# Performance work log

Hardware: AMD Instinct MI355X
Metric: run time of the kernel (lower is better)

Reference implementation:

```python
import jax, jax.numpy as jnp
import numpy as np

TEMP = 0.5
EPS_NORM = 1e-12  # F.normalize clamp eps
EPS_ROW = 1e-8


def _l2_normalize(x):
    n = jnp.sqrt(jnp.sum(x * x, axis=1, keepdims=True))
    return x / jnp.maximum(n, EPS_NORM)


def _sim(z1, z2):
    # exp(cosine_sim / T), [N, N]
    z1 = _l2_normalize(z1)
    z2 = _l2_normalize(z2)
    return jnp.exp(jnp.matmul(z1, z2.T) / TEMP)


def _loss_term(mat, pos):
    row = mat / (jnp.sum(mat, axis=1, keepdims=True) + EPS_ROW)
    return -jnp.mean(jnp.log(jnp.sum(row * pos, axis=-1)))


def setup_inputs() -> dict:
    key = jax.random.key(0)
    k1, k2, k3 = jax.random.split(key, 3)
    N, D = 8192, 64
    z_mp = jax.random.normal(k1, (N, D), dtype=jnp.float32)
    z_sc = jax.random.normal(k2, (N, D), dtype=jnp.float32)
    # sparse binary positive mask with guaranteed self-positives on diagonal
    pos = (jax.random.uniform(k3, (N, N)) < 0.005).astype(jnp.float32)
    pos = jnp.maximum(pos, jnp.eye(N, dtype=jnp.float32))
    return {"z_mp": z_mp, "z_sc": z_sc, "pos": pos}


def reference(z_mp, z_sc, pos):
    m_mp2sc = _sim(z_mp, z_sc)        # [N, N]
    m_sc2mp = m_mp2sc.T               # [N, N]
    m_mp2mp = _sim(z_mp, z_mp)        # [N, N]
    m_sc2sc = _sim(z_sc, z_sc)        # [N, N]
    loss = (_loss_term(m_mp2sc, pos)
            + _loss_term(m_sc2mp, pos)
            + _loss_term(m_mp2mp, pos)
            + _loss_term(m_sc2sc, pos))
    return loss
```

## Files before the change

kernel.cpp:

```cpp
#include <hip/hip_runtime.h>

#define N 8192
#define D 64
#define JSPLIT 16
#define JSTEPS (N / 64 / JSPLIT)

typedef unsigned short ushort_t;
typedef __attribute__((ext_vector_type(8))) short bf16x8;
typedef __attribute__((ext_vector_type(4))) float f32x4;

#define TWO_OVER_LN2 2.885390081777927f

#if __has_builtin(__builtin_amdgcn_exp2f)
#define EXP2F(x) __builtin_amdgcn_exp2f(x)
#else
#define EXP2F(x) exp2f(x)
#endif

typedef __attribute__((address_space(1))) const unsigned int g_u32;
typedef __attribute__((address_space(3))) unsigned int       l_u32;

__device__ inline ushort_t f32_to_bf16(float f) {
    union { float f; unsigned u; } c; c.f = f;
    unsigned r = (c.u + 0x7FFFu + ((c.u >> 16) & 1u)) >> 16;
    return (ushort_t)r;
}

__global__ void normalize_kernel(const float* __restrict__ z_mp,
                                 const float* __restrict__ z_sc,
                                 ushort_t* __restrict__ zn) {
    int lane = threadIdx.x & 63;
    int row  = blockIdx.x * 4 + (threadIdx.x >> 6);
    const float* src = (row < N) ? z_mp : z_sc;
    int srow = row & (N - 1);
    float x = src[srow * D + lane];
    float s = x * x;
    #pragma unroll
    for (int m = 32; m; m >>= 1) s += __shfl_xor(s, m, 64);
    float n = sqrtf(s);
    float scale = 1.0f / fmaxf(n, 1e-12f);
    zn[row * D + lane] = f32_to_bf16(x * scale);
}

__global__ __launch_bounds__(256, 2) void contrast_main(
        const ushort_t* __restrict__ zn,
        const float* __restrict__ pos,
        float* __restrict__ accum) {
    __shared__ float ptile[2][64 * 64];

    int lane = threadIdx.x & 63;
    int w    = threadIdx.x >> 6;
    int a = w >> 1, b = w & 1;
    int term = (a == 0) ? (b == 0 ? 2 : 0) : (b == 0 ? 1 : 3);
    int rq = lane >> 4;
    int lc = lane & 15;

    const ushort_t* Az = zn + a * (N * D);
    const ushort_t* Bz = zn + b * (N * D);

    int I0 = blockIdx.x * 64;
    int J0 = blockIdx.y * (N / JSPLIT);

    bf16x8 af[4][2];
    #pragma unroll
    for (int r = 0; r < 4; ++r)
        #pragma unroll
        for (int s = 0; s < 2; ++s)
            af[r][s] = *(const bf16x8*)(Az + (I0 + 16 * r + lc) * D + s * 32 + rq * 8);

    const ushort_t* bptr = Bz + ((size_t)(J0 + 4 * lc)) * D + rq * 8;
    const float*    sptr = pos + (size_t)(I0 + w * 16 + rq) * N + J0 + lc * 4;

    #define STAGE(bufv, jjv) do {                                              \
        float* dbase_ = &ptile[bufv][w * 16 * 64];                             \
        const float* sb_ = sptr + (size_t)(jjv) * 64;                          \
        _Pragma("unroll")                                                      \
        for (int it_ = 0; it_ < 4; ++it_) {                                    \
            __builtin_amdgcn_global_load_lds(                                  \
                (g_u32*)(sb_ + (size_t)it_ * 4 * N),                           \
                (l_u32*)(dbase_ + it_ * 4 * 64), 16, 0, 0);                    \
        }                                                                      \
    } while (0)

    bf16x8 bfc[4][2], bfn[4][2];

    float rs_acc[4][4], ps_acc[4][4];
    #pragma unroll
    for (int r = 0; r < 4; ++r)
        #pragma unroll
        for (int e = 0; e < 4; ++e) { rs_acc[r][e] = 0.0f; ps_acc[r][e] = 0.0f; }

    STAGE(0, 0);
    #pragma unroll
    for (int c = 0; c < 4; ++c)
        #pragma unroll
        for (int s = 0; s < 2; ++s)
            bfc[c][s] = *(const bf16x8*)(bptr + c * D + s * 32);
    __syncthreads();

    #pragma unroll 2
    for (int jj = 0; jj < JSTEPS; ++jj) {
        int buf = jj & 1;
        if (jj + 1 < JSTEPS) {
            STAGE(buf ^ 1, jj + 1);
            const ushort_t* bn = bptr + 64 * D;
            #pragma unroll
            for (int c = 0; c < 4; ++c)
                #pragma unroll
                for (int s = 0; s < 2; ++s)
                    bfn[c][s] = *(const bf16x8*)(bn + c * D + s * 32);
        }

        const float* tp = &ptile[buf][rq * 4 * 64 + lc * 4];

        #pragma unroll
        for (int r = 0; r < 4; ++r) {
            f32x4 acc[4];
            #pragma unroll
            for (int c = 0; c < 4; ++c) acc[c] = (f32x4){0.f, 0.f, 0.f, 0.f};
            #pragma unroll
            for (int s = 0; s < 2; ++s)
                #pragma unroll
                for (int c = 0; c < 4; ++c)
                    acc[c] = __builtin_amdgcn_mfma_f32_16x16x32_bf16(
                        af[r][s], bfc[c][s], acc[c], 0, 0, 0);

            #pragma unroll
            for (int e = 0; e < 4; ++e) {
                f32x4 p = *(const f32x4*)(tp + (16 * r + e) * 64);
                float rs = rs_acc[r][e], ps = ps_acc[r][e];
                #pragma unroll
                for (int c = 0; c < 4; ++c) {
                    float eV = EXP2F(acc[c][e] * TWO_OVER_LN2);
                    rs += eV;
                    ps = fmaf(eV, p[c], ps);
                }
                rs_acc[r][e] = rs; ps_acc[r][e] = ps;
            }
        }

        bptr += 64 * D;
        #pragma unroll
        for (int c = 0; c < 4; ++c)
            #pragma unroll
            for (int s = 0; s < 2; ++s)
                bfc[c][s] = bfn[c][s];
        __syncthreads();
    }
    #undef STAGE

    #pragma unroll
    for (int r = 0; r < 4; ++r)
        #pragma unroll
        for (int e = 0; e < 4; ++e) {
            float rs = rs_acc[r][e], ps = ps_acc[r][e];
            #pragma unroll
            for (int m = 1; m < 16; m <<= 1) {
                rs += __shfl_xor(rs, m, 64);
                ps += __shfl_xor(ps, m, 64);
            }
            rs_acc[r][e] = rs; ps_acc[r][e] = ps;
        }

    if (lc == 0) {
        #pragma unroll
        for (int r = 0; r < 4; ++r)
            #pragma unroll
            for (int e = 0; e < 4; ++e) {
                int gi = I0 + 16 * r + rq * 4 + e;
                atomicAdd(&accum[term * 2 * N + gi],     rs_acc[r][e]);
                atomicAdd(&accum[term * 2 * N + N + gi], ps_acc[r][e]);
            }
    }
}

__global__ void finalize_kernel(const float* __restrict__ accum,
                                float* __restrict__ out) {
    __shared__ float red[256];
    float local = 0.0f;
    for (int i = threadIdx.x; i < N; i += 256) {
        float s = 0.0f;
        #pragma unroll
        for (int t = 0; t < 4; ++t) {
            float rs = accum[t * 2 * N + i];
            float ps = accum[t * 2 * N + N + i];
            s += logf(ps / (rs + 1e-8f));
        }
        local += s;
    }
    red[threadIdx.x] = local;
    __syncthreads();
    for (int m = 128; m; m >>= 1) {
        if (threadIdx.x < m) red[threadIdx.x] += red[threadIdx.x + m];
        __syncthreads();
    }
    if (threadIdx.x == 0) out[0] = -red[0] / (float)N;
}

extern "C" void kernel_launch(void* const* d_in, const int* in_sizes, int n_in,
                              void* d_out, int out_size, void* d_ws, size_t ws_size,
                              hipStream_t stream) {
    const float* z_mp = (const float*)d_in[0];
    const float* z_sc = (const float*)d_in[1];
    const float* pos  = (const float*)d_in[2];
    float* out = (float*)d_out;

    ushort_t* zn = (ushort_t*)d_ws;
    float* accum = (float*)((char*)d_ws + (size_t)2 * N * D * sizeof(ushort_t));

    hipMemsetAsync(accum, 0, (size_t)4 * 2 * N * sizeof(float), stream);
    normalize_kernel<<<(2 * N) / 4, 256, 0, stream>>>(z_mp, z_sc, zn);
    dim3 grid(N / 64, JSPLIT);
    contrast_main<<<grid, 256, 0, stream>>>(zn, pos, accum);
    finalize_kernel<<<1, 256, 0, stream>>>(accum, out);
}
```

Before: 210.6 us.

## Compress positive mask to bitmask and fold exp scale into normalization

Adds a pre-pass that packs the dense float positive mask into 64-bit ballot bitmasks. The main kernel then reads 4-bit nibbles per lane from registers instead of staging float tiles through LDS with barriers. The sqrt(2/ln2) factor is folded into the normalized vectors so the exp2 argument needs no multiply. With no LDS, launch bounds rise to 4 blocks per CU. The dense 256MB mask is still read once by the compress pass, while main-kernel traffic and LDS synchronization shrink. Scaling before bf16 rounding slightly changes numerics.

```diff
diff --git a/kernel.cpp b/kernel.cpp
--- a/kernel.cpp
+++ b/kernel.cpp
@@ -9,16 +9,13 @@
 typedef __attribute__((ext_vector_type(8))) short bf16x8;
 typedef __attribute__((ext_vector_type(4))) float f32x4;
 
-#define TWO_OVER_LN2 2.885390081777927f
+#define SQRT_2_OVER_LN2 1.6986436f
 
 #if __has_builtin(__builtin_amdgcn_exp2f)
 #define EXP2F(x) __builtin_amdgcn_exp2f(x)
 #else
 #define EXP2F(x) exp2f(x)
 #endif
-
-typedef __attribute__((address_space(1))) const unsigned int g_u32;
-typedef __attribute__((address_space(3))) unsigned int       l_u32;
 
 __device__ inline ushort_t f32_to_bf16(float f) {
     union { float f; unsigned u; } c; c.f = f;
@@ -38,22 +35,41 @@
     #pragma unroll
     for (int m = 32; m; m >>= 1) s += __shfl_xor(s, m, 64);
     float n = sqrtf(s);
-    float scale = 1.0f / fmaxf(n, 1e-12f);
+    float scale = SQRT_2_OVER_LN2 / fmaxf(n, 1e-12f);
     zn[row * D + lane] = f32_to_bf16(x * scale);
 }
 
-__global__ __launch_bounds__(256, 2) void contrast_main(
+__global__ __launch_bounds__(256) void compress_kernel(
+        const float* __restrict__ pos,
+        unsigned long long* __restrict__ mask) {
+    int lane = threadIdx.x & 63;
+    size_t wv = (size_t)blockIdx.x * 4 + (threadIdx.x >> 6);
+    size_t nw = (size_t)gridDim.x * 4;
+    const size_t units = (size_t)N * N / 256;
+    for (size_t u = wv; u < units; u += nw) {
+        const float* base = pos + u * 256 + lane;
+        unsigned long long w0 = __ballot(base[0]   > 0.5f);
+        unsigned long long w1 = __ballot(base[64]  > 0.5f);
+        unsigned long long w2 = __ballot(base[128] > 0.5f);
+        unsigned long long w3 = __ballot(base[192] > 0.5f);
+        if (lane == 0) {
+            unsigned long long* mb = mask + u * 4;
+            mb[0] = w0; mb[1] = w1; mb[2] = w2; mb[3] = w3;
+        }
+    }
+}
+
+__global__ __launch_bounds__(256, 4) void contrast_main(
         const ushort_t* __restrict__ zn,
-        const float* __restrict__ pos,
+        const unsigned long long* __restrict__ mask,
         float* __restrict__ accum) {
-    __shared__ float ptile[2][64 * 64];
-
     int lane = threadIdx.x & 63;
     int w    = threadIdx.x >> 6;
     int a = w >> 1, b = w & 1;
     int term = (a == 0) ? (b == 0 ? 2 : 0) : (b == 0 ? 1 : 3);
     int rq = lane >> 4;
     int lc = lane & 15;
+    unsigned sh = (unsigned)lc * 4;
 
     const ushort_t* Az = zn + a * (N * D);
     const ushort_t* Bz = zn + b * (N * D);
@@ -69,20 +85,10 @@
             af[r][s] = *(const bf16x8*)(Az + (I0 + 16 * r + lc) * D + s * 32 + rq * 8);
 
     const ushort_t* bptr = Bz + ((size_t)(J0 + 4 * lc)) * D + rq * 8;
-    const float*    sptr = pos + (size_t)(I0 + w * 16 + rq) * N + J0 + lc * 4;
-
-    #define STAGE(bufv, jjv) do {                                              \
-        float* dbase_ = &ptile[bufv][w * 16 * 64];                             \
-        const float* sb_ = sptr + (size_t)(jjv) * 64;                          \
-        _Pragma("unroll")                                                      \
-        for (int it_ = 0; it_ < 4; ++it_) {                                    \
-            __builtin_amdgcn_global_load_lds(                                  \
-                (g_u32*)(sb_ + (size_t)it_ * 4 * N),                           \
-                (l_u32*)(dbase_ + it_ * 4 * 64), 16, 0, 0);                    \
-        }                                                                      \
-    } while (0)
+    const unsigned long long* mptr = mask + (size_t)(I0 + rq * 4) * (N / 64) + (J0 >> 6);
 
     bf16x8 bfc[4][2], bfn[4][2];
+    unsigned nc[16], nn[16];
 
     float rs_acc[4][4], ps_acc[4][4];
     #pragma unroll
@@ -90,28 +96,32 @@
         #pragma unroll
         for (int e = 0; e < 4; ++e) { rs_acc[r][e] = 0.0f; ps_acc[r][e] = 0.0f; }
 
-    STAGE(0, 0);
     #pragma unroll
     for (int c = 0; c < 4; ++c)
         #pragma unroll
         for (int s = 0; s < 2; ++s)
             bfc[c][s] = *(const bf16x8*)(bptr + c * D + s * 32);
-    __syncthreads();
+    #pragma unroll
+    for (int r = 0; r < 4; ++r)
+        #pragma unroll
+        for (int e = 0; e < 4; ++e)
+            nc[r * 4 + e] = (unsigned)(mptr[(16 * r + e) * (N / 64)] >> sh) & 0xFu;
 
     #pragma unroll 2
     for (int jj = 0; jj < JSTEPS; ++jj) {
-        int buf = jj & 1;
         if (jj + 1 < JSTEPS) {
-            STAGE(buf ^ 1, jj + 1);
             const ushort_t* bn = bptr + 64 * D;
             #pragma unroll
             for (int c = 0; c < 4; ++c)
                 #pragma unroll
                 for (int s = 0; s < 2; ++s)
                     bfn[c][s] = *(const bf16x8*)(bn + c * D + s * 32);
-        }
-
-        const float* tp = &ptile[buf][rq * 4 * 64 + lc * 4];
+            #pragma unroll
+            for (int r = 0; r < 4; ++r)
+                #pragma unroll
+                for (int e = 0; e < 4; ++e)
+                    nn[r * 4 + e] = (unsigned)(mptr[(16 * r + e) * (N / 64) + jj + 1] >> sh) & 0xFu;
+        }
 
         #pragma unroll
         for (int r = 0; r < 4; ++r) {
@@ -127,13 +137,13 @@
 
             #pragma unroll
             for (int e = 0; e < 4; ++e) {
-                f32x4 p = *(const f32x4*)(tp + (16 * r + e) * 64);
+                unsigned nib = nc[r * 4 + e];
                 float rs = rs_acc[r][e], ps = ps_acc[r][e];
                 #pragma unroll
                 for (int c = 0; c < 4; ++c) {
-                    float eV = EXP2F(acc[c][e] * TWO_OVER_LN2);
+                    float eV = EXP2F(acc[c][e]);
                     rs += eV;
-                    ps = fmaf(eV, p[c], ps);
+                    ps = fmaf((float)((nib >> c) & 1u), eV, ps);
                 }
                 rs_acc[r][e] = rs; ps_acc[r][e] = ps;
             }
@@ -145,9 +155,9 @@
             #pragma unroll
             for (int s = 0; s < 2; ++s)
                 bfc[c][s] = bfn[c][s];
-        __syncthreads();
-    }
-    #undef STAGE
+        #pragma unroll
+        for (int i = 0; i < 16; ++i) nc[i] = nn[i];
+    }
 
     #pragma unroll
     for (int r = 0; r < 4; ++r)
@@ -207,10 +217,13 @@
 
     ushort_t* zn = (ushort_t*)d_ws;
     float* accum = (float*)((char*)d_ws + (size_t)2 * N * D * sizeof(ushort_t));
+    unsigned long long* mask = (unsigned long long*)((char*)accum
+                               + (size_t)4 * 2 * N * sizeof(float));
 
     hipMemsetAsync(accum, 0, (size_t)4 * 2 * N * sizeof(float), stream);
     normalize_kernel<<<(2 * N) / 4, 256, 0, stream>>>(z_mp, z_sc, zn);
+    compress_kernel<<<2048, 256, 0, stream>>>(pos, mask);
     dim3 grid(N / 64, JSPLIT);
-    contrast_main<<<grid, 256, 0, stream>>>(zn, pos, accum);
+    contrast_main<<<grid, 256, 0, stream>>>(zn, mask, accum);
     finalize_kernel<<<1, 256, 0, stream>>>(accum, out);
 }
```

After: 700.0 us. +232.4%, slower.
